# Performance work log

Measured on AMD Instinct MI355X. Metric: run time of the kernel, lower is better.

Reference implementation:

```python
import jax, jax.numpy as jnp
import numpy as np

B = 16384
DENSE_IN = 512
N_SPARSE = 26
EMB = 128
OUT_DIM = 512
NI = N_SPARSE + 1  # 27 rows in interaction matrix
DOT_OUT = NI * (NI + 1) // 2 + DENSE_IN  # 378 + 512 = 890


def setup_inputs() -> dict:
    key = jax.random.key(0)
    ks = jax.random.split(key, 6)
    dense_tensor = jax.random.normal(ks[0], (B, DENSE_IN), dtype=jnp.float32)
    sparse_tensor = jax.random.normal(ks[1], (B, N_SPARSE, EMB), dtype=jnp.float32)
    # nn.Linear(DENSE_IN, EMB): weight [EMB, DENSE_IN], bias [EMB]
    Wp = jax.random.normal(ks[2], (EMB, DENSE_IN), dtype=jnp.float32) * (1.0 / np.sqrt(DENSE_IN))
    bp = jax.random.normal(ks[3], (EMB,), dtype=jnp.float32) * 0.01
    # nn.Linear(DOT_OUT, OUT_DIM): weight [OUT_DIM, DOT_OUT], bias [OUT_DIM]
    Wo = jax.random.normal(ks[4], (OUT_DIM, DOT_OUT), dtype=jnp.float32) * (1.0 / np.sqrt(DOT_OUT))
    bo = jax.random.normal(ks[5], (OUT_DIM,), dtype=jnp.float32) * 0.01
    return {"dense_tensor": dense_tensor, "sparse_tensor": sparse_tensor,
            "Wp": Wp, "bp": bp, "Wo": Wo, "bo": bo}


def reference(dense_tensor, sparse_tensor, Wp, bp, Wo, bo):
    # Project dense feature into embedding space (dims differ in this config)
    dense_proj = dense_tensor @ Wp.T + bp                      # [B, EMB]
    T = jnp.concatenate([dense_proj[:, None, :], sparse_tensor], axis=1)  # [B, NI, EMB]
    Z = jnp.einsum('bie,bje->bij', T, T)                       # [B, NI, NI]
    li, lj = jnp.tril_indices(NI)                              # include diagonal (offset=0)
    Zflat = Z[:, li, lj]                                       # [B, NI*(NI+1)/2]
    Zflat = jnp.concatenate([dense_tensor, Zflat], axis=-1)    # [B, DOT_OUT]
    out = Zflat @ Wo.T + bo                                    # [B, OUT_DIM]
    return out
```

## Files before the change

kernel.cpp:

```cpp
#include <hip/hip_runtime.h>

#define NB    16384
#define DIN   512
#define NSP   26
#define EMBD  128
#define NOUT  512
#define NI_   27
#define NTRI  378
#define DOTK  890
#define KPAD  896

typedef __attribute__((ext_vector_type(8)))  short bf16x8;
typedef __attribute__((ext_vector_type(4)))  float f32x4;

__device__ __forceinline__ short f2bf(float f) {
    unsigned u = __builtin_bit_cast(unsigned, f);
    unsigned r = (u + 0x7FFFu + ((u >> 16) & 1u)) >> 16;
    return (short)r;
}

__device__ __forceinline__ bf16x8 cvt8(float4 a, float4 b) {
    bf16x8 r;
    r[0] = f2bf(a.x); r[1] = f2bf(a.y); r[2] = f2bf(a.z); r[3] = f2bf(a.w);
    r[4] = f2bf(b.x); r[5] = f2bf(b.y); r[6] = f2bf(b.z); r[7] = f2bf(b.w);
    return r;
}

__device__ __forceinline__ void gld_lds16(const void* g, void* l) {
    __builtin_amdgcn_global_load_lds((const __attribute__((address_space(1))) void*)g,
                                     (__attribute__((address_space(3))) void*)l,
                                     16, 0, 0);
}

#define CONV_N   (NB * 128)
#define WOP_N    (NOUT * KPAD)
#define WPB_N    (EMBD * DIN)
__global__ __launch_bounds__(256) void prep_all_k(const float* __restrict__ dense,
                                                  const float* __restrict__ Wo,
                                                  const float* __restrict__ Wp,
                                                  short* __restrict__ zfb,
                                                  short* __restrict__ wop,
                                                  short* __restrict__ wpb) {
    int idx = blockIdx.x * 256 + threadIdx.x;
    if (idx < CONV_N) {
        int b = idx >> 7, c = (idx & 127) * 4;
        float4 v = *(const float4*)(dense + (size_t)b * DIN + c);
        unsigned lo = ((unsigned)(unsigned short)f2bf(v.y) << 16) | (unsigned short)f2bf(v.x);
        unsigned hi = ((unsigned)(unsigned short)f2bf(v.w) << 16) | (unsigned short)f2bf(v.z);
        int2 pk; pk.x = (int)lo; pk.y = (int)hi;
        *(int2*)(zfb + (size_t)b * KPAD + c) = pk;
    } else if (idx < CONV_N + WOP_N) {
        int j = idx - CONV_N;
        int o = j / KPAD, k = j - o * KPAD;
        wop[j] = (k < DOTK) ? f2bf(Wo[o * DOTK + k]) : (short)0;
    } else {
        int j = idx - CONV_N - WOP_N;
        if (j < WPB_N) wpb[j] = f2bf(Wp[j]);
    }
}

template <int BM, int BN, bool OUTBF>
__global__ __launch_bounds__(256) void gemm_mfma(const short* __restrict__ A, int lda,
                                                 const short* __restrict__ Bm, int ldb,
                                                 const float* __restrict__ bias,
                                                 void* __restrict__ Cp, int ldc, int K) {
    constexpr int WM = BM / 2, WN = BN / 2;
    constexpr int MT = WM / 16, NT = WN / 16;
    __shared__ short As[BM * 64];
    __shared__ short Bs[BN * 64];

    const int tid = threadIdx.x;
    const int w = tid >> 6, l = tid & 63;
    const int wm = w >> 1, wn = w & 1;
    const int r0 = l & 15, q = l >> 4;
    const int m0 = blockIdx.y * BM, n0 = blockIdx.x * BN;

    const int lr = l >> 3, pseg = l & 7;

    const f32x4 zero4 = {0.f, 0.f, 0.f, 0.f};
    f32x4 acc[MT][NT];
#pragma unroll
    for (int mi = 0; mi < MT; ++mi)
#pragma unroll
        for (int ni = 0; ni < NT; ++ni) acc[mi][ni] = zero4;

    for (int k0 = 0; k0 < K; k0 += 64) {
#pragma unroll
        for (int i = 0; i < BM / 32; ++i) {
            int r = w * (BM / 4) + i * 8 + lr;
            int ls = pseg ^ (r & 7);
            gld_lds16(A + (size_t)(m0 + r) * lda + k0 + ls * 8,
                      (char*)As + (w * (BM / 4) + i * 8) * 128);
        }
#pragma unroll
        for (int i = 0; i < BN / 32; ++i) {
            int r = w * (BN / 4) + i * 8 + lr;
            int ls = pseg ^ (r & 7);
            gld_lds16(Bm + (size_t)(n0 + r) * ldb + k0 + ls * 8,
                      (char*)Bs + (w * (BN / 4) + i * 8) * 128);
        }
        __syncthreads();

#pragma unroll
        for (int h = 0; h < 2; ++h) {
            bf16x8 af[MT], bfr[NT];
#pragma unroll
            for (int mi = 0; mi < MT; ++mi) {
                int r = wm * WM + mi * 16 + r0;
                af[mi] = *(const bf16x8*)&As[r * 64 + ((h * 4 + q) ^ (r & 7)) * 8];
            }
#pragma unroll
            for (int ni = 0; ni < NT; ++ni) {
                int r = wn * WN + ni * 16 + r0;
                bfr[ni] = *(const bf16x8*)&Bs[r * 64 + ((h * 4 + q) ^ (r & 7)) * 8];
            }
#pragma unroll
            for (int mi = 0; mi < MT; ++mi)
#pragma unroll
                for (int ni = 0; ni < NT; ++ni)
                    acc[mi][ni] = __builtin_amdgcn_mfma_f32_16x16x32_bf16(
                        af[mi], bfr[ni], acc[mi][ni], 0, 0, 0);
        }
        __syncthreads();
    }

#pragma unroll
    for (int mi = 0; mi < MT; ++mi) {
#pragma unroll
        for (int ni = 0; ni < NT; ++ni) {
            int col = n0 + wn * WN + ni * 16 + r0;
            float bb = bias[col];
#pragma unroll
            for (int r = 0; r < 4; ++r) {
                int row = m0 + wm * WM + mi * 16 + q * 4 + r;
                float v = acc[mi][ni][r] + bb;
                if (OUTBF) ((short*)Cp)[(size_t)row * ldc + col] = f2bf(v);
                else       ((float*)Cp)[(size_t)row * ldc + col] = v;
            }
        }
    }
}

__global__ __launch_bounds__(256) void interact_mfma(const float* __restrict__ sparse,
                                                     const short* __restrict__ dprojb,
                                                     short* __restrict__ zfb) {
    __shared__ short zt[4][NTRI];
    const int w = threadIdx.x >> 6, l = threadIdx.x & 63;
    const int b = blockIdx.x * 4 + w;
    const int r0 = l & 15, q = l >> 4;

    const float* srow = sparse + (size_t)b * (NSP * EMBD);
    const short* dp = dprojb + (size_t)b * EMBD;

    const f32x4 zero4 = {0.f, 0.f, 0.f, 0.f};
    f32x4 acc00 = zero4, acc10 = zero4, acc11 = zero4;

#pragma unroll
    for (int kc = 0; kc < 4; ++kc) {
        int k = kc * 32 + q * 8;
        bf16x8 f0, f1;
        if (r0 == 0) {
            f0 = *(const bf16x8*)(dp + k);
        } else {
            const float* p = srow + (size_t)(r0 - 1) * EMBD + k;
            f0 = cvt8(*(const float4*)p, *(const float4*)(p + 4));
        }
        if (r0 <= 10) {
            const float* p = srow + (size_t)(15 + r0) * EMBD + k;
            f1 = cvt8(*(const float4*)p, *(const float4*)(p + 4));
        } else {
            f1 = (bf16x8){0, 0, 0, 0, 0, 0, 0, 0};
        }
        acc00 = __builtin_amdgcn_mfma_f32_16x16x32_bf16(f0, f0, acc00, 0, 0, 0);
        acc10 = __builtin_amdgcn_mfma_f32_16x16x32_bf16(f1, f0, acc10, 0, 0, 0);
        acc11 = __builtin_amdgcn_mfma_f32_16x16x32_bf16(f1, f1, acc11, 0, 0, 0);
    }

#pragma unroll
    for (int r = 0; r < 4; ++r) {
        int row, col;
        row = q * 4 + r;       col = r0;
        if (col <= row)             zt[w][row * (row + 1) / 2 + col] = f2bf(acc00[r]);
        row = 16 + q * 4 + r;  col = r0;
        if (row < NI_)              zt[w][row * (row + 1) / 2 + col] = f2bf(acc10[r]);
               col = 16 + r0;
        if (row < NI_ && col <= row) zt[w][row * (row + 1) / 2 + col] = f2bf(acc11[r]);
    }
    __syncthreads();

    const int b0 = blockIdx.x * 4;
    for (int idx = threadIdx.x; idx < 4 * 384; idx += 256) {
        int rw = idx / 384, c = idx - rw * 384;
        short v = (c < NTRI) ? zt[rw][c] : (short)0;
        zfb[(size_t)(b0 + rw) * KPAD + DIN + c] = v;
    }
}

extern "C" void kernel_launch(void* const* d_in, const int* in_sizes, int n_in,
                              void* d_out, int out_size, void* d_ws, size_t ws_size,
                              hipStream_t stream) {
    const float* dense  = (const float*)d_in[0];
    const float* sparse = (const float*)d_in[1];
    const float* Wp     = (const float*)d_in[2];
    const float* bp     = (const float*)d_in[3];
    const float* Wo     = (const float*)d_in[4];
    const float* bo     = (const float*)d_in[5];
    float* out = (float*)d_out;

    short* zfb    = (short*)d_ws;
    short* dprojb = zfb + (size_t)NB * KPAD;
    short* wop    = dprojb + (size_t)NB * EMBD;
    short* wpb    = wop + (size_t)NOUT * KPAD;

    prep_all_k<<<(CONV_N + WOP_N + WPB_N + 255) / 256, 256, 0, stream>>>(
        dense, Wo, Wp, zfb, wop, wpb);

    gemm_mfma<128, 64, true><<<dim3(EMBD / 64, NB / 128), 256, 0, stream>>>(
        zfb, KPAD, wpb, DIN, bp, dprojb, EMBD, DIN);

    interact_mfma<<<NB / 4, 256, 0, stream>>>(sparse, dprojb, zfb);

    gemm_mfma<128, 128, false><<<dim3(NOUT / 128, NB / 128), 256, 0, stream>>>(
        zfb, KPAD, wop, KPAD, bo, out, NOUT, KPAD);
}
```

Before: 376.5 us.

## Vectorize prep conversions, swizzle GEMM block order, and simplify interaction writeback

The prep kernel now converts eight floats per thread with 16-byte bf16 stores instead of scalar or 8-byte stores. Both GEMMs remap block IDs so consecutive workgroups are spread across row tiles (an XCD-aware swizzle), and the projection GEMM uses smaller 64x64 tiles for more blocks. The interaction kernel drops the block-wide barrier, and each wave writes its own padded triangle row with 32-bit stores. These target instruction count, store width, cache locality across chiplets, and occupancy on the small projection GEMM. The swizzle assumes the workgroup count is divisible by 8.

After: 369.8 us. About the same (-1.8%).

```diff
diff --git a/kernel.cpp b/kernel.cpp
--- a/kernel.cpp
+++ b/kernel.cpp
@@ -32,9 +32,9 @@
                                      16, 0, 0);
 }
 
-#define CONV_N   (NB * 128)
-#define WOP_N    (NOUT * KPAD)
-#define WPB_N    (EMBD * DIN)
+#define CONV_N2  (NB * 64)
+#define WOP_N2   (NOUT * (KPAD / 8))
+#define WPB_N2   (EMBD * DIN / 8)
 __global__ __launch_bounds__(256) void prep_all_k(const float* __restrict__ dense,
                                                   const float* __restrict__ Wo,
                                                   const float* __restrict__ Wp,
@@ -42,24 +42,29 @@
                                                   short* __restrict__ wop,
                                                   short* __restrict__ wpb) {
     int idx = blockIdx.x * 256 + threadIdx.x;
-    if (idx < CONV_N) {
-        int b = idx >> 7, c = (idx & 127) * 4;
-        float4 v = *(const float4*)(dense + (size_t)b * DIN + c);
-        unsigned lo = ((unsigned)(unsigned short)f2bf(v.y) << 16) | (unsigned short)f2bf(v.x);
-        unsigned hi = ((unsigned)(unsigned short)f2bf(v.w) << 16) | (unsigned short)f2bf(v.z);
-        int2 pk; pk.x = (int)lo; pk.y = (int)hi;
-        *(int2*)(zfb + (size_t)b * KPAD + c) = pk;
-    } else if (idx < CONV_N + WOP_N) {
-        int j = idx - CONV_N;
-        int o = j / KPAD, k = j - o * KPAD;
-        wop[j] = (k < DOTK) ? f2bf(Wo[o * DOTK + k]) : (short)0;
+    if (idx < CONV_N2) {
+        int b = idx >> 6, c = (idx & 63) * 8;
+        const float4* p = (const float4*)(dense + (size_t)b * DIN + c);
+        *(bf16x8*)(zfb + (size_t)b * KPAD + c) = cvt8(p[0], p[1]);
+    } else if (idx < CONV_N2 + WOP_N2) {
+        int j = idx - CONV_N2;
+        int o = j / (KPAD / 8), rem = j - o * (KPAD / 8);
+        int k = rem * 8;
+        const float* src = Wo + (size_t)o * DOTK + k;
+        bf16x8 r;
+#pragma unroll
+        for (int t = 0; t < 8; ++t) r[t] = (k + t < DOTK) ? f2bf(src[t]) : (short)0;
+        *(bf16x8*)(wop + (size_t)o * KPAD + k) = r;
     } else {
-        int j = idx - CONV_N - WOP_N;
-        if (j < WPB_N) wpb[j] = f2bf(Wp[j]);
-    }
-}
-
-template <int BM, int BN, bool OUTBF>
+        int j = idx - CONV_N2 - WOP_N2;
+        if (j < WPB_N2) {
+            const float4* p = (const float4*)(Wp + (size_t)j * 8);
+            *(bf16x8*)(wpb + (size_t)j * 8) = cvt8(p[0], p[1]);
+        }
+    }
+}
+
+template <int BM, int BN, bool OUTBF, int GXL2>
 __global__ __launch_bounds__(256) void gemm_mfma(const short* __restrict__ A, int lda,
                                                  const short* __restrict__ Bm, int ldb,
                                                  const float* __restrict__ bias,
@@ -73,7 +78,12 @@
     const int w = tid >> 6, l = tid & 63;
     const int wm = w >> 1, wn = w & 1;
     const int r0 = l & 15, q = l >> 4;
-    const int m0 = blockIdx.y * BM, n0 = blockIdx.x * BN;
+
+    const int nwg = (int)(gridDim.y << GXL2);
+    const int bid = ((int)blockIdx.y << GXL2) | (int)blockIdx.x;
+    const int swz = (bid & 7) * (nwg >> 3) + (bid >> 3);
+    const int m0 = (swz >> GXL2) * BM;
+    const int n0 = (swz & ((1 << GXL2) - 1)) * BN;
 
     const int lr = l >> 3, pseg = l & 7;
 
@@ -144,7 +154,7 @@
 __global__ __launch_bounds__(256) void interact_mfma(const float* __restrict__ sparse,
                                                      const short* __restrict__ dprojb,
                                                      short* __restrict__ zfb) {
-    __shared__ short zt[4][NTRI];
+    __shared__ short zt[4][384];
     const int w = threadIdx.x >> 6, l = threadIdx.x & 63;
     const int b = blockIdx.x * 4 + w;
     const int r0 = l & 15, q = l >> 4;
@@ -186,14 +196,11 @@
                col = 16 + r0;
         if (row < NI_ && col <= row) zt[w][row * (row + 1) / 2 + col] = f2bf(acc11[r]);
     }
-    __syncthreads();
-
-    const int b0 = blockIdx.x * 4;
-    for (int idx = threadIdx.x; idx < 4 * 384; idx += 256) {
-        int rw = idx / 384, c = idx - rw * 384;
-        short v = (c < NTRI) ? zt[rw][c] : (short)0;
-        zfb[(size_t)(b0 + rw) * KPAD + DIN + c] = v;
-    }
+    if (l < 6) zt[w][NTRI + l] = 0;
+    const int* zrow = (const int*)zt[w];
+    int* dst = (int*)(zfb + (size_t)b * KPAD + DIN);
+#pragma unroll
+    for (int t = 0; t < 3; ++t) dst[t * 64 + l] = zrow[t * 64 + l];
 }
 
 extern "C" void kernel_launch(void* const* d_in, const int* in_sizes, int n_in,
@@ -212,14 +219,14 @@
     short* wop    = dprojb + (size_t)NB * EMBD;
     short* wpb    = wop + (size_t)NOUT * KPAD;
 
-    prep_all_k<<<(CONV_N + WOP_N + WPB_N + 255) / 256, 256, 0, stream>>>(
+    prep_all_k<<<(CONV_N2 + WOP_N2 + WPB_N2 + 255) / 256, 256, 0, stream>>>(
         dense, Wo, Wp, zfb, wop, wpb);
 
-    gemm_mfma<128, 64, true><<<dim3(EMBD / 64, NB / 128), 256, 0, stream>>>(
+    gemm_mfma<64, 64, true, 1><<<dim3(EMBD / 64, NB / 64), 256, 0, stream>>>(
         zfb, KPAD, wpb, DIN, bp, dprojb, EMBD, DIN);
 
     interact_mfma<<<NB / 4, 256, 0, stream>>>(sparse, dprojb, zfb);
 
-    gemm_mfma<128, 128, false><<<dim3(NOUT / 128, NB / 128), 256, 0, stream>>>(
+    gemm_mfma<128, 128, false, 2><<<dim3(NOUT / 128, NB / 128), 256, 0, stream>>>(
         zfb, KPAD, wop, KPAD, bo, out, NOUT, KPAD);
 }
```
